# Kernel optimization log

Measured on AMD Instinct MI355X. Metric: run time of the kernel, lower is better.

Reference implementation:

```python
import jax, jax.numpy as jnp
import numpy as np

L, B, D, H, R, C, WIN = 256, 64, 1024, 512, 8, 6, 10
N = B * L
DH = D + H  # concat(node_features, graph output)


def _window_pairs():
    pi, pk = [], []
    for j in range(L):
        for k in range(max(0, j - WIN), min(L, j + WIN + 1)):
            pi.append(j)
            pk.append(k)
    return np.asarray(pi, np.int32), np.asarray(pk, np.int32)


def setup_inputs() -> dict:
    key = jax.random.key(0)
    ks = jax.random.split(key, 16)
    s = 0.02
    pi, pk = _window_pairs()
    return {
        "features": jax.random.normal(ks[0], (L, B, D), jnp.float32),
        "Wscalar": jax.random.normal(ks[1], (D, L), jnp.float32) * s,   # MaskedEdgeAttention scalar
        "W_rel": jax.random.normal(ks[2], (R, D, H), jnp.float32) * s,  # RGCN per-relation weights
        "W_root": jax.random.normal(ks[3], (D, H), jnp.float32) * s,
        "b_rgcn": jnp.zeros((H,), jnp.float32),
        "W_nbr": jax.random.normal(ks[4], (H, H), jnp.float32) * s,     # GraphConv neighbor weight
        "W_self": jax.random.normal(ks[5], (H, H), jnp.float32) * s,
        "b_gc": jnp.zeros((H,), jnp.float32),
        "W_match": jax.random.normal(ks[6], (DH, DH), jnp.float32) * s,  # MatchingAttention 'general2'
        "b_match": jnp.zeros((DH,), jnp.float32),
        "W_lin": jax.random.normal(ks[7], (DH, H), jnp.float32) * s,
        "b_lin": jnp.zeros((H,), jnp.float32),
        "W_fc": jax.random.normal(ks[8], (H, C), jnp.float32) * s,
        "b_fc": jnp.zeros((C,), jnp.float32),
        "speakers": jax.random.randint(ks[9], (L, B), 0, 2, jnp.int32),
        "pair_i": jnp.asarray(pi),
        "pair_k": jnp.asarray(pk),
    }


def reference(features, Wscalar, W_rel, W_root, b_rgcn, W_nbr, W_self, b_gc,
              W_match, b_match, W_lin, b_lin, W_fc, b_fc,
              speakers, pair_i, pair_k):
    # --- edge attention scores (MaskedEdgeAttention, attn1 style) ---
    scale = jnp.einsum('sbd,dm->sbm', features, Wscalar)      # [L,B,L]
    alpha = jax.nn.softmax(scale, axis=0)
    alpha = jnp.transpose(alpha, (1, 2, 0))                   # [B, anchor, src]
    win = jnp.full((L, L), 1e-10, jnp.float32).at[pair_i, pair_k].set(1.0)
    masked = alpha * win
    scores = masked / jnp.sum(masked, axis=-1, keepdims=True)  # renormalized over window
    edge_norm = scores[:, pair_i, pair_k].reshape(-1)          # [E]

    # --- batch_graphify: flatten nodes conversation-major, build global edges ---
    x = jnp.transpose(features, (1, 0, 2)).reshape(N, D)       # [N, D]
    offs = jnp.arange(B, dtype=jnp.int32)[:, None] * L
    src = (offs + pair_i[None, :]).reshape(-1)
    dst = (offs + pair_k[None, :]).reshape(-1)
    sp = speakers.T                                            # [B, L]
    dir_bit = jnp.where(pair_i < pair_k, 0, 1).astype(jnp.int32)
    rel = (sp[:, pair_i] * 4 + sp[:, pair_k] * 2 + dir_bit[None, :]).reshape(-1)

    # --- RGCNConv: per-relation transform, edge_norm-weighted sum at dst + root ---
    h_all = jnp.einsum('nd,rdh->nrh', x, W_rel)                # [N, R, H]
    msg = h_all[src, rel] * edge_norm[:, None]                 # [E, H]
    agg = jax.ops.segment_sum(msg, dst, num_segments=N)
    h1 = agg + x @ W_root + b_rgcn

    # --- GraphConv: W_nbr @ sum_j x_j + W_self @ x + b ---
    nbr = jax.ops.segment_sum(h1[src], dst, num_segments=N)
    h2 = nbr @ W_nbr + h1 @ W_self + b_gc

    # --- attentive_node_features (MatchingAttention 'general2', full-length mask=1) ---
    em = jnp.concatenate([x, h2], axis=-1).reshape(B, L, DH)
    em = jnp.transpose(em, (1, 0, 2))                          # [L, B, DH] seq-major
    xt = jnp.einsum('tbd,de->tbe', em, W_match) + b_match
    a = jax.nn.softmax(jnp.tanh(jnp.einsum('tbe,sbe->bts', xt, em)), axis=2)
    att = jnp.einsum('bts,sbd->tbd', a, em)                    # [L, B, DH]

    # --- classify_node_features (dropout = eval identity) ---
    hidden = jax.nn.relu(jnp.einsum('tbd,dh->tbh', att, W_lin) + b_lin)
    logp = jax.nn.log_softmax(hidden @ W_fc + b_fc, axis=2)    # [L, B, C]
    return jnp.transpose(logp, (1, 0, 2)).reshape(N, C)
```

## Files before the change

### kernel.cpp

```cpp
#include <hip/hip_runtime.h>
#include <hip/hip_bf16.h>

#define Lc 256
#define Bc 64
#define Dc 1024
#define Hc 512
#define Rc 8
#define Cc 6
#define WINc 10
#define NWc 21
#define Nc (Bc*Lc)
#define DHc (Dc+Hc)
#define CH 8192

typedef __attribute__((ext_vector_type(8))) short short8;
typedef __attribute__((ext_vector_type(4))) float floatx4;

__device__ inline unsigned short f2b(float x) {
    __hip_bfloat16 h = __float2bfloat16(x);
    return *reinterpret_cast<unsigned short*>(&h);
}
__device__ inline float bf2f(unsigned short u) {
    __hip_bfloat16 h;
    *reinterpret_cast<unsigned short*>(&h) = u;
    return __bfloat162float(h);
}

__device__ inline long remap_row(int node) { return (long)(((node & 255) << 6) + (node >> 8)); }

typedef __attribute__((address_space(3))) unsigned int lds_u32;
typedef __attribute__((address_space(1))) unsigned int glb_u32;
__device__ inline void glds16(const unsigned short* g, unsigned short* l) {
    __builtin_amdgcn_global_load_lds((const glb_u32*)g, (lds_u32*)l, 16, 0, 0);
}

#define SB0 __builtin_amdgcn_sched_barrier(0)
#define BAR __builtin_amdgcn_s_barrier()

__global__ __launch_bounds__(256) void transpose_all(
    const float* __restrict__ Wscalar, const float* __restrict__ W_rel,
    const float* __restrict__ W_root, const float* __restrict__ W_nbr,
    const float* __restrict__ W_self, const float* __restrict__ W_match,
    const float* __restrict__ W_lin, unsigned short* __restrict__ WT)
{
    int t = blockIdx.x;
    const float* in; unsigned short* out; int N, ldo, n0, k0;
    if (t < 256) {
        in = Wscalar; out = WT; N = 256; ldo = 1024;
        n0 = (t & 7) * 32; k0 = (t >> 3) * 32;
    } else if (t < 4352) {
        int u = t - 256; int r = u >> 9; u &= 511;
        in = W_rel + (long)r * 524288; out = WT + 262144 + (long)r * 524288; N = 512; ldo = 1024;
        n0 = (u & 15) * 32; k0 = (u >> 4) * 32;
    } else if (t < 4864) {
        int u = t - 4352;
        in = W_root; out = WT + 262144 + 4096 * 1024; N = 512; ldo = 1024;
        n0 = (u & 15) * 32; k0 = (u >> 4) * 32;
    } else if (t < 5120) {
        int u = t - 4864;
        in = W_nbr; out = WT + 4980736; N = 512; ldo = 1024;
        n0 = (u & 15) * 32; k0 = (u >> 4) * 32;
    } else if (t < 5376) {
        int u = t - 5120;
        in = W_self; out = WT + 4980736 + 512; N = 512; ldo = 1024;
        n0 = (u & 15) * 32; k0 = (u >> 4) * 32;
    } else if (t < 7680) {
        int u = t - 5376;
        in = W_match; out = WT + 5505024; N = 1536; ldo = 1536;
        n0 = (u % 48) * 32; k0 = (u / 48) * 32;
    } else {
        int u = t - 7680;
        in = W_lin; out = WT + 7864320; N = 512; ldo = 1536;
        n0 = (u & 15) * 32; k0 = (u >> 4) * 32;
    }
    __shared__ float tt[32][33];
    int tx = threadIdx.x & 31, ty = threadIdx.x >> 5;
    #pragma unroll
    for (int i = 0; i < 4; i++) tt[ty + i * 8][tx] = in[(long)(k0 + ty + i * 8) * N + n0 + tx];
    __syncthreads();
    #pragma unroll
    for (int i = 0; i < 4; i++) out[(long)(n0 + ty + i * 8) * ldo + k0 + tx] = f2b(tt[tx][ty + i * 8]);
}

__global__ __launch_bounds__(256) void partition_kernel(const int* __restrict__ spk,
        int* __restrict__ idx, int* __restrict__ cnts)
{
    int c = blockIdx.x;
    int tid = threadIdx.x;
    int base = c * CH;
    __shared__ int zs[256];
    int zcount = 0;
    for (int i = 0; i < CH / 256; i++) {
        int n = base + tid * (CH / 256) + i;
        if (spk[(n & 255) * 64 + (n >> 8)] == 0) zcount++;
    }
    zs[tid] = zcount; __syncthreads();
    for (int off = 1; off < 256; off <<= 1) {
        int v = (tid >= off) ? zs[tid - off] : 0;
        __syncthreads();
        zs[tid] += v;
        __syncthreads();
    }
    int Z = zs[255];
    int zpos = zs[tid] - zcount;
    int opos = tid * (CH / 256) - zpos;
    for (int i = 0; i < CH / 256; i++) {
        int nl = tid * (CH / 256) + i;
        int n = base + nl;
        if (spk[(n & 255) * 64 + (n >> 8)] == 0) idx[base + (zpos++)] = nl;
        else                                     idx[base + Z + (opos++)] = nl;
    }
    if (tid == 0) cnts[c] = Z;
}

__global__ __launch_bounds__(256) void build_em_x(const float* __restrict__ feats,
                                                  unsigned short* __restrict__ em)
{
    int n = blockIdx.x;
    int tid = threadIdx.x;
    const float* f = feats + remap_row(n) * Dc;
    float4 v = ((const float4*)f)[tid];
    unsigned short* e = em + (long)n * DHc + tid * 4;
    e[0] = f2b(v.x); e[1] = f2b(v.y); e[2] = f2b(v.z); e[3] = f2b(v.w);
}

template<bool CBF, bool CT, bool BIAS, bool RELU>
__global__ __launch_bounds__(256) void gemm_as(
    const unsigned short* __restrict__ A, const unsigned short* __restrict__ B,
    void* __restrict__ Cv, const float* __restrict__ bias,
    int K, int lda, int ldb, int ldc, long sA, long sB, long sC)
{
    __shared__ __align__(16) unsigned short As[4096];
    __shared__ __align__(16) unsigned short Bs[4096];
    const int tid = threadIdx.x;
    const int z = blockIdx.z;
    const int m0 = blockIdx.y * 128, n0 = blockIdx.x * 128;
    const int lane = tid & 63, wave = tid >> 6;
    const int q = lane >> 4, mr = lane & 15;
    const int wrow = (wave >> 1) * 64, wcol = (wave & 1) * 64;

    const unsigned short* Ag0 = A + z * sA + (long)(m0 + wave * 32 + mr) * lda + q * 8;
    const unsigned short* Ag1 = Ag0 + (long)16 * lda;
    const unsigned short* Bg0 = B + z * sB + (long)(n0 + wave * 32 + mr) * ldb + q * 8;
    const unsigned short* Bg1 = Bg0 + (long)16 * ldb;
    unsigned short* Al0 = As + wave * 1024;
    unsigned short* Bl0 = Bs + wave * 1024;

    floatx4 acc[4][4];
    #pragma unroll
    for (int mt = 0; mt < 4; mt++)
        #pragma unroll
        for (int nt = 0; nt < 4; nt++) acc[mt][nt] = (floatx4){0.f, 0.f, 0.f, 0.f};

    const int ga = (wave >> 1) * 2048;
    const int gb = (wave & 1) * 2048;

    for (int k0 = 0; k0 < K; k0 += 32) {
        glds16(Ag0 + k0, Al0);
        glds16(Ag1 + k0, Al0 + 512);
        glds16(Bg0 + k0, Bl0);
        glds16(Bg1 + k0, Bl0 + 512);
        __syncthreads();
        short8 af[4], bfr[4];
        #pragma unroll
        for (int t = 0; t < 4; t++) {
            af[t]  = *(const short8*)&As[ga + t * 512 + lane * 8];
            bfr[t] = *(const short8*)&Bs[gb + t * 512 + lane * 8];
        }
        #pragma unroll
        for (int mt = 0; mt < 4; mt++)
            #pragma unroll
            for (int nt = 0; nt < 4; nt++)
                acc[mt][nt] = __builtin_amdgcn_mfma_f32_16x16x32_bf16(af[mt], bfr[nt], acc[mt][nt], 0, 0, 0);
        __syncthreads();
    }

    float* Cf = (float*)Cv;
    unsigned short* Cb = (unsigned short*)Cv;
    #pragma unroll
    for (int mt = 0; mt < 4; mt++) {
        #pragma unroll
        for (int nt = 0; nt < 4; nt++) {
            int col = n0 + wcol + nt * 16 + mr;
            float bv = BIAS ? bias[col] : 0.f;
            #pragma unroll
            for (int rg = 0; rg < 4; rg++) {
                int row = m0 + wrow + mt * 16 + q * 4 + rg;
                float v = acc[mt][nt][rg] + bv;
                if (RELU) v = fmaxf(v, 0.f);
                if (CT) {
                    Cb[(long)(row >> 8) * 131072 + (long)col * 256 + (row & 255)] = f2b(v);
                } else {
                    long ci = z * sC + (long)row * ldc + col;
                    if (CBF) Cb[ci] = f2b(v);
                    else     Cf[ci] = v;
                }
            }
        }
    }
}

__device__ __forceinline__ void gemm256_loop(
    unsigned short* lp,
    const unsigned short* Ag0, const unsigned short* Ag1,
    const unsigned short* Bg0, const unsigned short* Bg1,
    int NT, int wofs, const int* offA, const int* offB, floatx4 (&acc)[8][4])
{
    glds16(Ag0,      lp + wofs);                 glds16(Ag1,      lp + 4096 + wofs);
    glds16(Bg0,      lp + 32768 + wofs);         glds16(Bg1,      lp + 32768 + 4096 + wofs);
    glds16(Ag0 + 32, lp + 8192 + wofs);          glds16(Ag1 + 32, lp + 8192 + 4096 + wofs);
    glds16(Bg0 + 32, lp + 32768 + 8192 + wofs);  glds16(Bg1 + 32, lp + 32768 + 8192 + 4096 + wofs);
    glds16(Ag0 + 64, lp + 16384 + wofs);         glds16(Ag1 + 64, lp + 16384 + 4096 + wofs);
    glds16(Bg0 + 64, lp + 32768 + 16384 + wofs); glds16(Bg1 + 64, lp + 32768 + 16384 + 4096 + wofs);
    asm volatile("s_waitcnt vmcnt(4)" ::: "memory");
    SB0; BAR; SB0;

    for (int t = 0; t < NT; t++) {
        const int buf = t & 1;
        const int ab  = buf * 16384;
        short8 aF[4], bF[4];

        #pragma unroll
        for (int i = 0; i < 4; i++) aF[i] = *(const short8*)(lp + ab + offA[i]);
        #pragma unroll
        for (int i = 0; i < 4; i++) bF[i] = *(const short8*)(lp + 32768 + ab + offB[i]);
        if (t + 1 < NT) {
            const int kc = (t + 1) * 64 + 32;
            unsigned short* d = lp + (buf ^ 1) * 16384 + 8192 + wofs;
            glds16(Ag0 + kc, d); glds16(Ag1 + kc, d + 4096);
        }
        SB0; BAR; SB0;
        asm volatile("s_waitcnt lgkmcnt(0)" ::: "memory"); SB0;
        __builtin_amdgcn_s_setprio(1);
        #pragma unroll
        for (int mt = 0; mt < 4; mt++)
            #pragma unroll
            for (int nt = 0; nt < 4; nt++)
                acc[mt][nt] = __builtin_amdgcn_mfma_f32_16x16x32_bf16(aF[mt], bF[nt], acc[mt][nt], 0, 0, 0);
        __builtin_amdgcn_s_setprio(0);
        SB0; BAR; SB0;

        #pragma unroll
        for (int i = 0; i < 4; i++) aF[i] = *(const short8*)(lp + ab + offA[4 + i]);
        if (t + 1 < NT) {
            const int kc = (t + 1) * 64 + 32;
            unsigned short* d = lp + 32768 + (buf ^ 1) * 16384 + 8192 + wofs;
            glds16(Bg0 + kc, d); glds16(Bg1 + kc, d + 4096);
        }
        SB0; BAR; SB0;
        asm volatile("s_waitcnt lgkmcnt(0)" ::: "memory"); SB0;
        __builtin_amdgcn_s_setprio(1);
        #pragma unroll
        for (int mt = 0; mt < 4; mt++)
            #pragma unroll
            for (int nt = 0; nt < 4; nt++)
                acc[4 + mt][nt] = __builtin_amdgcn_mfma_f32_16x16x32_bf16(aF[mt], bF[nt], acc[4 + mt][nt], 0, 0, 0);
        __builtin_amdgcn_s_setprio(0);
        SB0; BAR; SB0;

        #pragma unroll
        for (int i = 0; i < 4; i++) aF[i] = *(const short8*)(lp + ab + 8192 + offA[i]);
        #pragma unroll
        for (int i = 0; i < 4; i++) bF[i] = *(const short8*)(lp + 32768 + ab + 8192 + offB[i]);
        if (t + 2 < NT) {
            const int kc = (t + 2) * 64;
            unsigned short* d = lp + buf * 16384 + wofs;
            glds16(Ag0 + kc, d); glds16(Ag1 + kc, d + 4096);
        }
        SB0; BAR; SB0;
        asm volatile("s_waitcnt lgkmcnt(0)" ::: "memory"); SB0;
        __builtin_amdgcn_s_setprio(1);
        #pragma unroll
        for (int mt = 0; mt < 4; mt++)
            #pragma unroll
            for (int nt = 0; nt < 4; nt++)
                acc[mt][nt] = __builtin_amdgcn_mfma_f32_16x16x32_bf16(aF[mt], bF[nt], acc[mt][nt], 0, 0, 0);
        __builtin_amdgcn_s_setprio(0);
        SB0; BAR; SB0;

        #pragma unroll
        for (int i = 0; i < 4; i++) aF[i] = *(const short8*)(lp + ab + 8192 + offA[4 + i]);
        if (t + 2 < NT) {
            const int kc = (t + 2) * 64;
            unsigned short* d = lp + 32768 + buf * 16384 + wofs;
            glds16(Bg0 + kc, d); glds16(Bg1 + kc, d + 4096);
        }
        if (t < NT - 2)       { asm volatile("s_waitcnt vmcnt(4)" ::: "memory"); }
        else if (t == NT - 2) { asm volatile("s_waitcnt vmcnt(0)" ::: "memory"); }
        SB0; BAR; SB0;
        asm volatile("s_waitcnt lgkmcnt(0)" ::: "memory"); SB0;
        __builtin_amdgcn_s_setprio(1);
        #pragma unroll
        for (int mt = 0; mt < 4; mt++)
            #pragma unroll
            for (int nt = 0; nt < 4; nt++)
                acc[4 + mt][nt] = __builtin_amdgcn_mfma_f32_16x16x32_bf16(aF[mt], bF[nt], acc[4 + mt][nt], 0, 0, 0);
        __builtin_amdgcn_s_setprio(0);
        SB0; BAR; SB0;
    }
}

__device__ __forceinline__ void frag_offsets(int wm, int wn, int q, int mr, int* offA, int* offB)
{
    #pragma unroll
    for (int mt = 0; mt < 8; mt++) {
        int row = wm * 128 + mt * 16 + mr;
        offA[mt] = row * 32 + ((q ^ ((row >> 1) & 3)) * 8);
    }
    #pragma unroll
    for (int nt = 0; nt < 4; nt++) {
        int row = wn * 64 + nt * 16 + mr;
        offB[nt] = row * 32 + ((q ^ ((row >> 1) & 3)) * 8);
    }
}

template<bool CBF, bool CT, bool BIAS, bool RELU>
__global__ __launch_bounds__(512, 2) void gemm256(
    const unsigned short* __restrict__ A, const unsigned short* __restrict__ B,
    void* __restrict__ Cv, const float* __restrict__ bias,
    int K, int lda, int ldb, int ldc)
{
    __shared__ __align__(16) unsigned short LDS[65536];
    unsigned short* lp = &LDS[0];
    const int tid  = threadIdx.x;
    const int lane = tid & 63, wave = tid >> 6;
    const int wm = wave >> 2, wn = wave & 3;
    const int m0 = blockIdx.y * 256, n0 = blockIdx.x * 256;
    const int NT = K >> 6;
    const int q = lane >> 4, mr = lane & 15;

    const int r0 = wave * 16 + (lane >> 2);
    const int r1 = r0 + 128;
    const int c0 = ((lane & 3) ^ ((r0 >> 1) & 3)) * 8;
    const int c1 = ((lane & 3) ^ ((r1 >> 1) & 3)) * 8;
    const unsigned short* Ag0 = A + (long)(m0 + r0) * lda + c0;
    const unsigned short* Ag1 = A + (long)(m0 + r1) * lda + c1;
    const unsigned short* Bg0 = B + (long)(n0 + r0) * ldb + c0;
    const unsigned short* Bg1 = B + (long)(n0 + r1) * ldb + c1;
    const int wofs = wave * 512;

    int offA[8], offB[4];
    frag_offsets(wm, wn, q, mr, offA, offB);

    floatx4 acc[8][4];
    #pragma unroll
    for (int mt = 0; mt < 8; mt++)
        #pragma unroll
        for (int nt = 0; nt < 4; nt++) acc[mt][nt] = (floatx4){0.f, 0.f, 0.f, 0.f};

    gemm256_loop(lp, Ag0, Ag1, Bg0, Bg1, NT, wofs, offA, offB, acc);

    float* Cf = (float*)Cv;
    unsigned short* Cb = (unsigned short*)Cv;
    #pragma unroll
    for (int mt = 0; mt < 8; mt++) {
        #pragma unroll
        for (int nt = 0; nt < 4; nt++) {
            int col = n0 + wn * 64 + nt * 16 + mr;
            float bv = BIAS ? bias[col] : 0.f;
            #pragma unroll
            for (int rg = 0; rg < 4; rg++) {
                int row = m0 + wm * 128 + mt * 16 + q * 4 + rg;
                float v = acc[mt][nt][rg] + bv;
                if (RELU) v = fmaxf(v, 0.f);
                if (CT) {
                    Cb[(long)(row >> 8) * 131072 + (long)col * 256 + (row & 255)] = f2b(v);
                } else {
                    long ci = (long)row * ldc + col;
                    if (CBF) Cb[ci] = f2b(v);
                    else     Cf[ci] = v;
                }
            }
        }
    }
}

__global__ __launch_bounds__(512, 2) void rgcn256(
    const unsigned short* __restrict__ A, const unsigned short* __restrict__ B,
    unsigned short* __restrict__ C, const int* __restrict__ idx,
    const int* __restrict__ cntp)
{
    const int cnt0 = *cntp;
    const int t0 = (cnt0 + 255) >> 8;
    const int M1 = CH - cnt0;
    const int t1 = (M1 + 255) >> 8;
    const int ty = blockIdx.y;
    int sblk, m0, M, off;
    if (ty < t0)           { sblk = 0; m0 = ty << 8;        M = cnt0; off = 0; }
    else if (ty < t0 + t1) { sblk = 1; m0 = (ty - t0) << 8; M = M1;   off = cnt0; }
    else return;

    const int x = blockIdx.x;
    const int brow = ((x < 8) ? sblk * 2048 : 2048) + x * 256;

    __shared__ __align__(16) unsigned short LDS[65536];
    unsigned short* lp = &LDS[0];
    const int tid  = threadIdx.x;
    const int lane = tid & 63, wave = tid >> 6;
    const int wm = wave >> 2, wn = wave & 3;
    const int q = lane >> 4, mr = lane & 15;

    const int r0 = wave * 16 + (lane >> 2);
    const int r1 = r0 + 128;
    const int c0 = ((lane & 3) ^ ((r0 >> 1) & 3)) * 8;
    const int c1 = ((lane & 3) ^ ((r1 >> 1) & 3)) * 8;
    const int gr0 = idx[off + min(m0 + r0, M - 1)];
    const int gr1 = idx[off + min(m0 + r1, M - 1)];
    const unsigned short* Ag0 = A + (long)gr0 * DHc + c0;
    const unsigned short* Ag1 = A + (long)gr1 * DHc + c1;
    const unsigned short* Bg0 = B + (long)(brow + r0) * 1024 + c0;
    const unsigned short* Bg1 = B + (long)(brow + r1) * 1024 + c1;
    const int wofs = wave * 512;

    int offA[8], offB[4];
    frag_offsets(wm, wn, q, mr, offA, offB);

    floatx4 acc[8][4];
    #pragma unroll
    for (int mt = 0; mt < 8; mt++)
        #pragma unroll
        for (int nt = 0; nt < 4; nt++) acc[mt][nt] = (floatx4){0.f, 0.f, 0.f, 0.f};

    gemm256_loop(lp, Ag0, Ag1, Bg0, Bg1, 16 , wofs, offA, offB, acc);

    #pragma unroll
    for (int mt = 0; mt < 8; mt++) {
        int rowb = m0 + wm * 128 + mt * 16 + q * 4;
        int cr[4];
        #pragma unroll
        for (int rg = 0; rg < 4; rg++) cr[rg] = idx[off + min(rowb + rg, M - 1)];
        #pragma unroll
        for (int nt = 0; nt < 4; nt++) {
            int col = x * 256 + wn * 64 + nt * 16 + mr;
            #pragma unroll
            for (int rg = 0; rg < 4; rg++)
                C[(long)cr[rg] * 2560 + col] = f2b(acc[mt][nt][rg]);
        }
    }
}

__global__ __launch_bounds__(512, 2) void gemm256_mw(
    const unsigned short* __restrict__ A, const unsigned short* __restrict__ B,
    unsigned short* __restrict__ xt, unsigned short* __restrict__ emWT,
    const float* __restrict__ b_match, const float* __restrict__ b_lin)
{
    __shared__ __align__(16) unsigned short LDS[65536];
    unsigned short* lp = &LDS[0];
    const int tid  = threadIdx.x;
    const int lane = tid & 63, wave = tid >> 6;
    const int wm = wave >> 2, wn = wave & 3;
    const int m0 = blockIdx.y * 256, n0 = blockIdx.x * 256;
    const int q = lane >> 4, mr = lane & 15;

    const int r0 = wave * 16 + (lane >> 2);
    const int r1 = r0 + 128;
    const int c0 = ((lane & 3) ^ ((r0 >> 1) & 3)) * 8;
    const int c1 = ((lane & 3) ^ ((r1 >> 1) & 3)) * 8;
    const unsigned short* Ag0 = A + (long)(m0 + r0) * DHc + c0;
    const unsigned short* Ag1 = A + (long)(m0 + r1) * DHc + c1;
    const unsigned short* Bg0 = B + (long)(n0 + r0) * 1536 + c0;
    const unsigned short* Bg1 = B + (long)(n0 + r1) * 1536 + c1;
    const int wofs = wave * 512;

    int offA[8], offB[4];
    frag_offsets(wm, wn, q, mr, offA, offB);

    floatx4 acc[8][4];
    #pragma unroll
    for (int mt = 0; mt < 8; mt++)
        #pragma unroll
        for (int nt = 0; nt < 4; nt++) acc[mt][nt] = (floatx4){0.f, 0.f, 0.f, 0.f};

    gemm256_loop(lp, Ag0, Ag1, Bg0, Bg1, 24 , wofs, offA, offB, acc);

    if (n0 < 1536) {
        #pragma unroll
        for (int mt = 0; mt < 8; mt++) {
            #pragma unroll
            for (int nt = 0; nt < 4; nt++) {
                int col = n0 + wn * 64 + nt * 16 + mr;
                float bv = b_match[col];
                #pragma unroll
                for (int rg = 0; rg < 4; rg++) {
                    int row = m0 + wm * 128 + mt * 16 + q * 4 + rg;
                    xt[(long)row * DHc + col] = f2b(acc[mt][nt][rg] + bv);
                }
            }
        }
    } else {
        #pragma unroll
        for (int mt = 0; mt < 8; mt++) {
            #pragma unroll
            for (int nt = 0; nt < 4; nt++) {
                int col = (n0 - 1536) + wn * 64 + nt * 16 + mr;
                float bv = b_lin[col];
                #pragma unroll
                for (int rg = 0; rg < 4; rg++) {
                    int row = m0 + wm * 128 + mt * 16 + q * 4 + rg;
                    emWT[(long)(row >> 8) * 131072 + (long)col * 256 + (row & 255)] =
                        f2b(acc[mt][nt][rg] + bv);
                }
            }
        }
    }
}

__global__ __launch_bounds__(256) void edge_norm_kernel(const float* __restrict__ scale,
                                                        float* __restrict__ enorm)
{
    int g = blockIdx.x * 256 + threadIdx.x;
    int b = g >> 8, j = g & 255;
    int klo = max(0, j - WINc), khi = min(Lc - 1, j + WINc);
    float vals[NWc];
    float m = -1e30f;
    for (int k = klo; k <= khi; k++) {
        float v = scale[(long)((b << 8) + k) * Lc + j];
        vals[k - klo] = v;
        m = fmaxf(m, v);
    }
    float s = 0.f;
    for (int k = klo; k <= khi; k++) {
        float e = expf(vals[k - klo] - m);
        vals[k - klo] = e;
        s += e;
    }
    float inv = 1.f / s;
    for (int k = klo; k <= khi; k++)
        enorm[(long)g * NWc + (k - j + WINc)] = vals[k - klo] * inv;
}

__global__ __launch_bounds__(256) void rgcn_gather4(const unsigned short* __restrict__ hall4,
        const float* __restrict__ enorm, const int* __restrict__ spk,
        const float* __restrict__ b_rgcn, float* __restrict__ h1, int chunk_base)
{
    int nloc = blockIdx.x;
    int n = chunk_base + nloc;
    int b = n >> 8, k = n & 255;
    int tid = threadIdx.x;
    int spkk = spk[k * 64 + b];
    int jlo = max(0, k - WINc), jhi = min(Lc - 1, k + WINc);
    unsigned int ru = *(const unsigned int*)(hall4 + (long)nloc * 2560 + 2048 + 2 * tid);
    float a0 = bf2f((unsigned short)(ru & 0xffff)) + b_rgcn[2 * tid];
    float a1 = bf2f((unsigned short)(ru >> 16)) + b_rgcn[2 * tid + 1];
    int cb = spkk * 2;
    for (int j = jlo; j <= jhi; j++) {
        int c = cb + ((j < k) ? 0 : 1);
        float w = enorm[((long)((b << 8) + j)) * NWc + (k - j + WINc)];
        unsigned int u = *(const unsigned int*)(hall4 + ((long)(nloc - k + j)) * 2560 + c * 512 + 2 * tid);
        a0 += w * bf2f((unsigned short)(u & 0xffff));
        a1 += w * bf2f((unsigned short)(u >> 16));
    }
    *(float2*)&h1[(long)n * Hc + 2 * tid] = make_float2(a0, a1);
}

__global__ __launch_bounds__(256) void build_anh1(const float* __restrict__ h1,
                                                  unsigned short* __restrict__ anh1)
{
    int n = blockIdx.x;
    int b = n >> 8, k = n & 255;
    int tid = threadIdx.x;
    int jlo = max(0, k - WINc), jhi = min(Lc - 1, k + WINc);
    float a0 = 0.f, a1 = 0.f;
    for (int j = jlo; j <= jhi; j++) {
        const float* src = h1 + ((long)((b << 8) + j)) * Hc;
        a0 += src[tid];
        a1 += src[tid + 256];
    }
    unsigned short* dst = anh1 + (long)n * 1024;
    const float* self = h1 + (long)n * Hc;
    dst[tid]       = f2b(a0);
    dst[tid + 256] = f2b(a1);
    dst[tid + 512] = f2b(self[tid]);
    dst[tid + 768] = f2b(self[tid + 256]);
}

__global__ __launch_bounds__(256) void tanh_softmax_rows(const float* __restrict__ S,
                                                         unsigned short* __restrict__ a)
{
    int row = blockIdx.x;
    int tid = threadIdx.x;
    __shared__ float red[256];
    float v = tanhf(S[(long)row * Lc + tid]);
    red[tid] = v; __syncthreads();
    for (int s = 128; s > 0; s >>= 1) { if (tid < s) red[tid] = fmaxf(red[tid], red[tid + s]); __syncthreads(); }
    float m = red[0]; __syncthreads();
    float e = expf(v - m);
    red[tid] = e; __syncthreads();
    for (int s = 128; s > 0; s >>= 1) { if (tid < s) red[tid] += red[tid + s]; __syncthreads(); }
    float sum = red[0];
    a[(long)row * Lc + tid] = f2b(e / sum);
}

__global__ __launch_bounds__(256) void out_kernel(const unsigned short* __restrict__ hidden,
        const float* __restrict__ Wfc, const float* __restrict__ bfc, float* __restrict__ out)
{
    int tid = threadIdx.x;
    int lane = tid & 63;
    int row = blockIdx.x * 4 + (tid >> 6);
    float acc[Cc] = {};
    const unsigned short* h = hidden + (long)row * Hc;
    for (int k = lane; k < Hc; k += 64) {
        float hv = bf2f(h[k]);
        #pragma unroll
        for (int c = 0; c < Cc; c++) acc[c] += hv * Wfc[k * Cc + c];
    }
    #pragma unroll
    for (int c = 0; c < Cc; c++)
        for (int off = 32; off > 0; off >>= 1) acc[c] += __shfl_down(acc[c], off, 64);
    if (lane == 0) {
        float m = -1e30f;
        #pragma unroll
        for (int c = 0; c < Cc; c++) { acc[c] += bfc[c]; m = fmaxf(m, acc[c]); }
        float s = 0.f;
        #pragma unroll
        for (int c = 0; c < Cc; c++) s += expf(acc[c] - m);
        float lse = logf(s);
        #pragma unroll
        for (int c = 0; c < Cc; c++) out[(long)row * Cc + c] = acc[c] - m - lse;
    }
}

extern "C" void kernel_launch(void* const* d_in, const int* in_sizes, int n_in,
                              void* d_out, int out_size, void* d_ws, size_t ws_size,
                              hipStream_t stream)
{
    const float* feats   = (const float*)d_in[0];
    const float* Wscalar = (const float*)d_in[1];
    const float* W_rel   = (const float*)d_in[2];
    const float* W_root  = (const float*)d_in[3];
    const float* b_rgcn  = (const float*)d_in[4];
    const float* W_nbr   = (const float*)d_in[5];
    const float* W_self  = (const float*)d_in[6];
    const float* b_gc    = (const float*)d_in[7];
    const float* W_match = (const float*)d_in[8];
    const float* b_match = (const float*)d_in[9];
    const float* W_lin   = (const float*)d_in[10];
    const float* b_lin   = (const float*)d_in[11];
    const float* W_fc    = (const float*)d_in[12];
    const float* b_fc    = (const float*)d_in[13];
    const int*   spk     = (const int*)d_in[14];

    char* wsb = (char*)d_ws;
    unsigned short* em    = (unsigned short*)wsb;
    char* RB = wsb + 50331648;
    float*          scale = (float*)RB;
    unsigned short* hall4 = (unsigned short*)RB;
    unsigned short* anh1  = (unsigned short*)RB;
    unsigned short* xt    = (unsigned short*)RB;
    unsigned short* hidden= (unsigned short*)(RB + 16777216);
    char* HB = wsb + 100663296;
    float*          h1    = (float*)HB;
    float*          S     = (float*)HB;
    unsigned short* emWT  = (unsigned short*)(wsb + 117440512);
    int* idx              = (int*)(HB + 16777216);
    int* cnts             = (int*)(HB + 16777216 + 65536);
    unsigned short* WT    = (unsigned short*)(wsb + 134217728);
    unsigned short* WscalarT = WT;
    unsigned short* WrelT    = WT + 262144;
    unsigned short* WgcT     = WT + 4980736;
    unsigned short* WmatchT  = WT + 5505024;
    unsigned short* ac    = (unsigned short*)(wsb + 134217728);
    float*          enorm = (float*)(wsb + 151519232);

    transpose_all<<<dim3(8448), 256, 0, stream>>>(Wscalar, W_rel, W_root, W_nbr, W_self,
                                                  W_match, W_lin, WT);
    partition_kernel<<<dim3(2), 256, 0, stream>>>(spk, idx, cnts);
    build_em_x<<<dim3(Nc), 256, 0, stream>>>(feats, em);

    gemm_as<false, false, false, false><<<dim3(2, 128, 1), 256, 0, stream>>>(
        em, WscalarT, scale, nullptr, 1024, DHc, 1024, 256, 0, 0, 0);

    edge_norm_kernel<<<dim3(64), 256, 0, stream>>>(scale, enorm);

    for (int c = 0; c < 2; c++) {
        const unsigned short* emc = em + (long)c * CH * DHc;
        rgcn256<<<dim3(10, 33, 1), 512, 0, stream>>>(
            emc, WrelT, hall4, idx + c * CH, cnts + c);
        rgcn_gather4<<<dim3(CH), 256, 0, stream>>>(hall4, enorm, spk, b_rgcn, h1, c * CH);
    }

    build_anh1<<<dim3(Nc), 256, 0, stream>>>(h1, anh1);
    gemm256<true, false, true, false><<<dim3(2, 64, 1), 512, 0, stream>>>(
        anh1, WgcT, em + 1024, b_gc, 1024, 1024, 1024, DHc);

    gemm256_mw<<<dim3(8, 64, 1), 512, 0, stream>>>(
        em, WmatchT, xt, emWT, b_match, b_lin);

    gemm_as<false, false, false, false><<<dim3(2, 2, 64), 256, 0, stream>>>(
        xt, em, S, nullptr, DHc, DHc, DHc, 256, 393216, 393216, 65536);

    tanh_softmax_rows<<<dim3(Nc), 256, 0, stream>>>(S, ac);

    gemm_as<true, false, false, true><<<dim3(4, 2, 64), 256, 0, stream>>>(
        ac, emWT, hidden, nullptr, 256, 256, 256, 512, 65536, 131072, 131072);

    out_kernel<<<dim3(Nc / 4), 256, 0, stream>>>(hidden, W_fc, b_fc, (float*)d_out);
}
```

Measured before the change: 717.6 us.

## Prefetch LDS fragments one stage ahead and remap blocks across XCDs

The 256x256 GEMM main loop now double-buffers its register fragments. It issues the LDS reads for the next MFMA group before the barrier and drops the explicit lgkmcnt(0) waits, so LDS latency overlaps with the MFMA work. Separately, the three 256-tile GEMM kernels remap block IDs so that consecutive logical tiles land on the same XCD, which should improve L2 reuse. The cost is more live VGPRs for the extra fragment buffers, and the code now relies on the compiler inserting correct waits before each use.

```diff
diff --git a/kernel.cpp b/kernel.cpp
--- a/kernel.cpp
+++ b/kernel.cpp
@@ -36,6 +36,17 @@
 
 #define SB0 __builtin_amdgcn_sched_barrier(0)
 #define BAR __builtin_amdgcn_s_barrier()
+
+__device__ __forceinline__ void xcd_remap(int gridX, int& x, int& y)
+{
+    int nwg = gridDim.x * gridDim.y;
+    int bid = blockIdx.y * gridDim.x + blockIdx.x;
+    int q = nwg >> 3, r = nwg & 7;
+    int xcd = bid & 7, pos = bid >> 3;
+    int logical = xcd * q + min(xcd, r) + pos;
+    x = logical % gridX;
+    y = logical / gridX;
+}
 
 __global__ __launch_bounds__(256) void transpose_all(
     const float* __restrict__ Wscalar, const float* __restrict__ W_rel,
@@ -200,6 +211,13 @@
     }
 }
 
+#define MFMA16(ACCBASE, AFR, BFR) \
+    { _Pragma("unroll") \
+      for (int mt = 0; mt < 4; mt++) \
+        _Pragma("unroll") \
+        for (int nt = 0; nt < 4; nt++) \
+            acc[ACCBASE + mt][nt] = __builtin_amdgcn_mfma_f32_16x16x32_bf16(AFR[mt], BFR[nt], acc[ACCBASE + mt][nt], 0, 0, 0); }
+
 __device__ __forceinline__ void gemm256_loop(
     unsigned short* lp,
     const unsigned short* Ag0, const unsigned short* Ag1,
@@ -215,71 +233,57 @@
     asm volatile("s_waitcnt vmcnt(4)" ::: "memory");
     SB0; BAR; SB0;
 
+    short8 aQ[4], a2Q[4], bQ[4], b2Q[4];
+    #pragma unroll
+    for (int i = 0; i < 4; i++) aQ[i] = *(const short8*)(lp + offA[i]);
+    #pragma unroll
+    for (int i = 0; i < 4; i++) bQ[i] = *(const short8*)(lp + 32768 + offB[i]);
+
     for (int t = 0; t < NT; t++) {
         const int buf = t & 1;
         const int ab  = buf * 16384;
-        short8 aF[4], bF[4];
-
-        #pragma unroll
-        for (int i = 0; i < 4; i++) aF[i] = *(const short8*)(lp + ab + offA[i]);
-        #pragma unroll
-        for (int i = 0; i < 4; i++) bF[i] = *(const short8*)(lp + 32768 + ab + offB[i]);
+
         if (t + 1 < NT) {
             const int kc = (t + 1) * 64 + 32;
             unsigned short* d = lp + (buf ^ 1) * 16384 + 8192 + wofs;
             glds16(Ag0 + kc, d); glds16(Ag1 + kc, d + 4096);
         }
+        #pragma unroll
+        for (int i = 0; i < 4; i++) a2Q[i] = *(const short8*)(lp + ab + offA[4 + i]);
         SB0; BAR; SB0;
-        asm volatile("s_waitcnt lgkmcnt(0)" ::: "memory"); SB0;
         __builtin_amdgcn_s_setprio(1);
-        #pragma unroll
-        for (int mt = 0; mt < 4; mt++)
-            #pragma unroll
-            for (int nt = 0; nt < 4; nt++)
-                acc[mt][nt] = __builtin_amdgcn_mfma_f32_16x16x32_bf16(aF[mt], bF[nt], acc[mt][nt], 0, 0, 0);
+        MFMA16(0, aQ, bQ)
         __builtin_amdgcn_s_setprio(0);
         SB0; BAR; SB0;
 
-        #pragma unroll
-        for (int i = 0; i < 4; i++) aF[i] = *(const short8*)(lp + ab + offA[4 + i]);
         if (t + 1 < NT) {
             const int kc = (t + 1) * 64 + 32;
             unsigned short* d = lp + 32768 + (buf ^ 1) * 16384 + 8192 + wofs;
             glds16(Bg0 + kc, d); glds16(Bg1 + kc, d + 4096);
         }
+        #pragma unroll
+        for (int i = 0; i < 4; i++) aQ[i]  = *(const short8*)(lp + ab + 8192 + offA[i]);
+        #pragma unroll
+        for (int i = 0; i < 4; i++) b2Q[i] = *(const short8*)(lp + 32768 + ab + 8192 + offB[i]);
         SB0; BAR; SB0;
-        asm volatile("s_waitcnt lgkmcnt(0)" ::: "memory"); SB0;
         __builtin_amdgcn_s_setprio(1);
-        #pragma unroll
-        for (int mt = 0; mt < 4; mt++)
-            #pragma unroll
-            for (int nt = 0; nt < 4; nt++)
-                acc[4 + mt][nt] = __builtin_amdgcn_mfma_f32_16x16x32_bf16(aF[mt], bF[nt], acc[4 + mt][nt], 0, 0, 0);
+        MFMA16(4, a2Q, bQ)
         __builtin_amdgcn_s_setprio(0);
         SB0; BAR; SB0;
 
-        #pragma unroll
-        for (int i = 0; i < 4; i++) aF[i] = *(const short8*)(lp + ab + 8192 + offA[i]);
-        #pragma unroll
-        for (int i = 0; i < 4; i++) bF[i] = *(const short8*)(lp + 32768 + ab + 8192 + offB[i]);
         if (t + 2 < NT) {
             const int kc = (t + 2) * 64;
             unsigned short* d = lp + buf * 16384 + wofs;
             glds16(Ag0 + kc, d); glds16(Ag1 + kc, d + 4096);
         }
+        #pragma unroll
+        for (int i = 0; i < 4; i++) a2Q[i] = *(const short8*)(lp + ab + 8192 + offA[4 + i]);
         SB0; BAR; SB0;
-        asm volatile("s_waitcnt lgkmcnt(0)" ::: "memory"); SB0;
         __builtin_amdgcn_s_setprio(1);
-        #pragma unroll
-        for (int mt = 0; mt < 4; mt++)
-            #pragma unroll
-            for (int nt = 0; nt < 4; nt++)
-                acc[mt][nt] = __builtin_amdgcn_mfma_f32_16x16x32_bf16(aF[mt], bF[nt], acc[mt][nt], 0, 0, 0);
+        MFMA16(0, aQ, b2Q)
         __builtin_amdgcn_s_setprio(0);
         SB0; BAR; SB0;
 
-        #pragma unroll
-        for (int i = 0; i < 4; i++) aF[i] = *(const short8*)(lp + ab + 8192 + offA[4 + i]);
         if (t + 2 < NT) {
             const int kc = (t + 2) * 64;
             unsigned short* d = lp + 32768 + buf * 16384 + wofs;
@@ -288,13 +292,16 @@
         if (t < NT - 2)       { asm volatile("s_waitcnt vmcnt(4)" ::: "memory"); }
         else if (t == NT - 2) { asm volatile("s_waitcnt vmcnt(0)" ::: "memory"); }
         SB0; BAR; SB0;
-        asm volatile("s_waitcnt lgkmcnt(0)" ::: "memory"); SB0;
+        if (t + 1 < NT) {
+            const int ab2 = (buf ^ 1) * 16384;
+            #pragma unroll
+            for (int i = 0; i < 4; i++) aQ[i] = *(const short8*)(lp + ab2 + offA[i]);
+            #pragma unroll
+            for (int i = 0; i < 4; i++) bQ[i] = *(const short8*)(lp + 32768 + ab2 + offB[i]);
+        }
+        SB0;
         __builtin_amdgcn_s_setprio(1);
-        #pragma unroll
-        for (int mt = 0; mt < 4; mt++)
-            #pragma unroll
-            for (int nt = 0; nt < 4; nt++)
-                acc[4 + mt][nt] = __builtin_amdgcn_mfma_f32_16x16x32_bf16(aF[mt], bF[nt], acc[4 + mt][nt], 0, 0, 0);
+        MFMA16(4, a2Q, b2Q)
         __builtin_amdgcn_s_setprio(0);
         SB0; BAR; SB0;
     }
@@ -325,7 +332,9 @@
     const int tid  = threadIdx.x;
     const int lane = tid & 63, wave = tid >> 6;
     const int wm = wave >> 2, wn = wave & 3;
-    const int m0 = blockIdx.y * 256, n0 = blockIdx.x * 256;
+    int bx, by;
+    xcd_remap(gridDim.x, bx, by);
+    const int m0 = by * 256, n0 = bx * 256;
     const int NT = K >> 6;
     const int q = lane >> 4, mr = lane & 15;
 
@@ -384,13 +393,13 @@
     const int t0 = (cnt0 + 255) >> 8;
     const int M1 = CH - cnt0;
     const int t1 = (M1 + 255) >> 8;
-    const int ty = blockIdx.y;
+    int x, ty;
+    xcd_remap(gridDim.x, x, ty);
     int sblk, m0, M, off;
     if (ty < t0)           { sblk = 0; m0 = ty << 8;        M = cnt0; off = 0; }
     else if (ty < t0 + t1) { sblk = 1; m0 = (ty - t0) << 8; M = M1;   off = cnt0; }
     else return;
 
-    const int x = blockIdx.x;
     const int brow = ((x < 8) ? sblk * 2048 : 2048) + x * 256;
 
     __shared__ __align__(16) unsigned short LDS[65536];
@@ -449,7 +458,9 @@
     const int tid  = threadIdx.x;
     const int lane = tid & 63, wave = tid >> 6;
     const int wm = wave >> 2, wn = wave & 3;
-    const int m0 = blockIdx.y * 256, n0 = blockIdx.x * 256;
+    int bx, by;
+    xcd_remap(gridDim.x, bx, by);
+    const int m0 = by * 256, n0 = bx * 256;
     const int q = lane >> 4, mr = lane & 15;
 
     const int r0 = wave * 16 + (lane >> 2);
```

Result: no change. 707.8 us (-1.4%).
